# Optimization experiments

Hardware: AMD Instinct MI355X
Metric: run time of the kernel (lower is better)

## Reference

```python
import jax, jax.numpy as jnp
import numpy as np

N = 50000
E = 600000
FEAT = 32
ACT = 8
H = 128
HEADS = 4
C = H // HEADS
L = 3
NEG_SLOPE = 0.2
LN_EPS = 1e-5


def setup_inputs() -> dict:
    key = jax.random.key(0)
    ks = jax.random.split(key, 32)
    s = 0.05
    inp = {
        'x': jax.random.normal(ks[0], (N, FEAT), jnp.float32),
        'action': jax.random.normal(ks[1], (N, ACT), jnp.float32),
        'edge_index': jax.random.randint(ks[2], (2, E), 0, N, jnp.int32),
        # node encoder: Linear(feat+act -> H) + LayerNorm
        'W0': jax.random.normal(ks[3], (FEAT + ACT, H), jnp.float32) * s,
        'b0': jnp.zeros((H,), jnp.float32),
        'ln0_g': jnp.ones((H,), jnp.float32),
        'ln0_b': jnp.zeros((H,), jnp.float32),
        # GAT layers (stacked over L): lin W [L,H,heads*C], att vectors, bias, LayerNorm
        'Wg': jax.random.normal(ks[4], (L, H, HEADS * C), jnp.float32) * s,
        'att_src': jax.random.normal(ks[5], (L, HEADS, C), jnp.float32) * s,
        'att_dst': jax.random.normal(ks[6], (L, HEADS, C), jnp.float32) * s,
        'bg': jnp.zeros((L, HEADS * C), jnp.float32),
        'lng_g': jnp.ones((L, H), jnp.float32),
        'lng_b': jnp.zeros((L, H), jnp.float32),
        # dynamics head
        'Wd1': jax.random.normal(ks[7], (H, H), jnp.float32) * s,
        'bd1': jnp.zeros((H,), jnp.float32),
        'Wd2': jax.random.normal(ks[8], (H, FEAT), jnp.float32) * s,
        'bd2': jnp.zeros((FEAT,), jnp.float32),
        # reward head
        'Wr1': jax.random.normal(ks[9], (H, H // 2), jnp.float32) * s,
        'br1': jnp.zeros((H // 2,), jnp.float32),
        'Wr2': jax.random.normal(ks[10], (H // 2, 1), jnp.float32) * s,
        'br2': jnp.zeros((1,), jnp.float32),
        # constraint head
        'Wc1': jax.random.normal(ks[11], (H, H // 2), jnp.float32) * s,
        'bc1': jnp.zeros((H // 2,), jnp.float32),
        'Wc2': jax.random.normal(ks[12], (H // 2, 1), jnp.float32) * s,
        'bc2': jnp.zeros((1,), jnp.float32),
    }
    return inp


def _layernorm(x, g, b):
    mu = jnp.mean(x, axis=-1, keepdims=True)
    var = jnp.mean(jnp.square(x - mu), axis=-1, keepdims=True)
    return (x - mu) * jax.lax.rsqrt(var + LN_EPS) * g + b


def _gat_layer(h, src, dst, W, a_src, a_dst, bias):
    # PyG GATConv: xp = lin(h) per head; alpha = leaky_relu(a_src.x_j + a_dst.x_i)
    xp = (h @ W).reshape(N, HEADS, C)                    # [N, heads, C]
    s_src = jnp.sum(xp * a_src, axis=-1)                 # [N, heads]
    s_dst = jnp.sum(xp * a_dst, axis=-1)                 # [N, heads]
    alpha = jax.nn.leaky_relu(s_src[src] + s_dst[dst], NEG_SLOPE)  # [E', heads]
    # segment softmax over edges grouped by destination node
    amax = jax.ops.segment_max(alpha, dst, num_segments=N)
    ex = jnp.exp(alpha - amax[dst])
    den = jax.ops.segment_sum(ex, dst, num_segments=N)
    attn = ex / den[dst]                                 # [E', heads]
    msg = xp[src] * attn[..., None]                      # [E', heads, C]
    out = jax.ops.segment_sum(msg.reshape(-1, HEADS * C), dst, num_segments=N)
    return out + bias                                    # [N, H]


def reference(x, action, edge_index, W0, b0, ln0_g, ln0_b, Wg, att_src, att_dst,
              bg, lng_g, lng_b, Wd1, bd1, Wd2, bd2, Wr1, br1, Wr2, br2,
              Wc1, bc1, Wc2, bc2):
    # add self loops (PyG GATConv default)
    loops = jnp.arange(N, dtype=edge_index.dtype)
    src = jnp.concatenate([edge_index[0], loops])
    dst = jnp.concatenate([edge_index[1], loops])

    h = jax.nn.relu(_layernorm(jnp.concatenate([x, action], axis=-1) @ W0 + b0, ln0_g, ln0_b))
    for l in range(L):
        h_new = _gat_layer(h, src, dst, Wg[l], att_src[l], att_dst[l], bg[l])
        h_new = jax.nn.relu(_layernorm(h_new, lng_g[l], lng_b[l]))
        h = h + h_new

    delta_x = jax.nn.relu(h @ Wd1 + bd1) @ Wd2 + bd2
    next_x = x + delta_x
    graph_emb = jnp.mean(h, axis=0, keepdims=True)       # global_mean_pool, single graph
    reward = (jax.nn.relu(graph_emb @ Wr1 + br1) @ Wr2 + br2).squeeze(-1)
    constraint_prob = jax.nn.sigmoid(jax.nn.relu(graph_emb @ Wc1 + bc1) @ Wc2 + bc2).squeeze(-1)
    return delta_x, next_x, reward, constraint_prob
```

## Files before the change

kernel.cpp:

```cpp
#include <hip/hip_runtime.h>

typedef unsigned short u16;
typedef __attribute__((ext_vector_type(8))) short bf16x8;
typedef __attribute__((ext_vector_type(4))) float f32x4;

#define NN 50000
#define EE 600000
#define EP 650000
#define LNEPS 1e-5f
#define ENCB 1563
#define HB 2344
#define CNTB 2540
#define WTOT 93858
#define BSWN 65536
#define CW 64

__device__ __forceinline__ float bf2f(u16 u) {
    union { unsigned int i; float f; } v; v.i = ((unsigned int)u) << 16; return v.f;
}
__device__ __forceinline__ u16 f2bf(float f) {
    union { float f; unsigned int i; } v; v.f = f;
    unsigned int x = v.i;
    unsigned int r = x + 0x7fffu + ((x >> 16) & 1u);
    return (u16)(r >> 16);
}
__device__ __forceinline__ float ldf(const void* p, long i, int bf) {
    return bf ? bf2f(((const u16*)p)[i]) : ((const float*)p)[i];
}
__device__ __forceinline__ void stf(void* p, long i, int bf, float v) {
    if (bf) ((u16*)p)[i] = f2bf(v); else ((float*)p)[i] = v;
}

struct P22 { const void* p[22]; };

__global__ __launch_bounds__(256) void init7(P22 w, float* __restrict__ wf,
                                             u16* __restrict__ bsw,
                                             int* __restrict__ deg,
                                             float* __restrict__ gacc,
                                             int* __restrict__ flag) {
    const unsigned w0 = *(const unsigned*)w.p[2];
    const int bf = (w0 == 0x3F803F80u) ? 1 : 0;
    int i = blockIdx.x * 256 + threadIdx.x;
    if (i < WTOT) {
        const int offs[23] = {0,5120,5248,5376,5504,54656,55040,55424,55808,56192,56576,
                              72960,73088,77184,77216,85408,85472,85536,85537,93729,93793,
                              93857,93858};
        int seg = 0;
        while (offs[seg + 1] <= i) ++seg;
        wf[i] = ldf(w.p[seg], i - offs[seg], bf);
        return;
    }
    i -= WTOT;
    if (i < BSWN) {
        int mat = i >> 14, rem = i & 16383;
        int ct = rem >> 11, r2 = rem & 2047;
        int kb = r2 >> 9, r3 = r2 & 511;
        int lane = r3 >> 3, j = r3 & 7;
        int k = kb * 32 + (lane >> 4) * 8 + j;
        int n = ct * 16 + (lane & 15);
        float v = (mat < 3) ? ldf(w.p[4], (long)mat * 16384 + (long)k * 128 + n, bf)
                            : ldf(w.p[10], (long)k * 128 + n, bf);
        bsw[i] = f2bf(v);
        return;
    }
    i -= BSWN;
    if (i < NN) { deg[i] = 0; return; }
    i -= NN;
    if (i < 2048) { gacc[i] = 0.f; return; }
    if (i == 2048) *flag = bf;
}

__global__ __launch_bounds__(256) void enc9(
    const void* __restrict__ x, const void* __restrict__ act,
    const float* __restrict__ wf, u16* __restrict__ hb,
    const int* __restrict__ flg, const int* __restrict__ ei,
    int* __restrict__ deg, int* __restrict__ rank) {
    if (blockIdx.x >= ENCB) {
        int e = (blockIdx.x - ENCB) * 256 + threadIdx.x;
        if (e < EE) {
            int d = ei[EE + e];
            rank[e] = atomicAdd(&deg[d], 1);
        }
        return;
    }
    const float* W0f = wf;
    const float* b0f = wf + 5120;
    const float* gf  = wf + 5248;
    const float* bbf = wf + 5376;
    __shared__ float As[32][41];
    const int bf = *flg;
    int t = threadIdx.x;
    int r0 = blockIdx.x * 32;
    #pragma unroll
    for (int i = 0; i < 5; ++i) {
        int idx = t + i * 256;
        int r = idx / 40, k = idx - r * 40;
        int rr = r0 + r; if (rr >= NN) rr = NN - 1;
        As[r][k] = (k < 32) ? ldf(x, (long)rr * 32 + k, bf)
                            : ldf(act, (long)rr * 8 + (k - 32), bf);
    }
    __syncthreads();
    int colq = t & 31, mq = t >> 5;
    int col0 = colq * 4;
    float4 b0v = *(const float4*)(b0f + col0);
    float acc[4][4];
    #pragma unroll
    for (int j = 0; j < 4; ++j) {
        acc[j][0] = b0v.x; acc[j][1] = b0v.y; acc[j][2] = b0v.z; acc[j][3] = b0v.w;
    }
    #pragma unroll 2
    for (int k = 0; k < 40; ++k) {
        float4 b4 = *(const float4*)(W0f + k * 128 + col0);
        float a0 = As[mq * 4 + 0][k];
        float a1 = As[mq * 4 + 1][k];
        float a2 = As[mq * 4 + 2][k];
        float a3 = As[mq * 4 + 3][k];
        acc[0][0] += a0 * b4.x; acc[0][1] += a0 * b4.y; acc[0][2] += a0 * b4.z; acc[0][3] += a0 * b4.w;
        acc[1][0] += a1 * b4.x; acc[1][1] += a1 * b4.y; acc[1][2] += a1 * b4.z; acc[1][3] += a1 * b4.w;
        acc[2][0] += a2 * b4.x; acc[2][1] += a2 * b4.y; acc[2][2] += a2 * b4.z; acc[2][3] += a2 * b4.w;
        acc[3][0] += a3 * b4.x; acc[3][1] += a3 * b4.y; acc[3][2] += a3 * b4.z; acc[3][3] += a3 * b4.w;
    }
    float4 gv = *(const float4*)(gf + col0);
    float4 bv = *(const float4*)(bbf + col0);
    #pragma unroll
    for (int j = 0; j < 4; ++j) {
        int row = r0 + mq * 4 + j;
        float pa = acc[j][0] + acc[j][1] + acc[j][2] + acc[j][3];
        #pragma unroll
        for (int o = 1; o <= 16; o <<= 1) pa += __shfl_xor(pa, o, 32);
        float mu = pa * (1.f / 128.f);
        float d0 = acc[j][0] - mu, d1 = acc[j][1] - mu;
        float d2 = acc[j][2] - mu, d3 = acc[j][3] - mu;
        float q = d0 * d0 + d1 * d1 + d2 * d2 + d3 * d3;
        #pragma unroll
        for (int o = 1; o <= 16; o <<= 1) q += __shfl_xor(q, o, 32);
        float rs = rsqrtf(q * (1.f / 128.f) + LNEPS);
        if (row < NN) {
            ushort4 hbv;
            hbv.x = f2bf(fmaxf(d0 * rs * gv.x + bv.x, 0.f));
            hbv.y = f2bf(fmaxf(d1 * rs * gv.y + bv.y, 0.f));
            hbv.z = f2bf(fmaxf(d2 * rs * gv.z + bv.z, 0.f));
            hbv.w = f2bf(fmaxf(d3 * rs * gv.w + bv.w, 0.f));
            *(ushort4*)(hb + (long)row * 128 + col0) = hbv;
        }
    }
}

__global__ __launch_bounds__(256) void lin_score(
    const u16* __restrict__ hb, const u16* __restrict__ bswm,
    u16* __restrict__ out, const float* __restrict__ wf, int layer,
    float* __restrict__ s_src, float* __restrict__ s_dst,
    int doscatter, const int* __restrict__ ei, const int* __restrict__ rank,
    const int* __restrict__ deg, int* __restrict__ csrc) {
    if (doscatter && blockIdx.x >= ENCB) {
        int e = (blockIdx.x - ENCB) * 256 + threadIdx.x;
        if (e < EP) {
            if (e < EE) {
                int sv = ei[e], d = ei[EE + e];
                csrc[(long)d * CW + rank[e]] = sv;
            } else {
                int n = e - EE;
                csrc[(long)n * CW + deg[n]] = n;
            }
        }
        return;
    }
    __shared__ u16 As[32 * 136];
    int t = threadIdx.x;
    int r0 = blockIdx.x * 32;
    #pragma unroll
    for (int i = 0; i < 2; ++i) {
        int idx = (t + i * 256) * 8;
        int r = idx >> 7, k = idx & 127;
        int rr = r0 + r; if (rr >= NN) rr = NN - 1;
        int4 v = *(const int4*)(hb + (long)rr * 128 + k);
        *(int4*)(As + r * 136 + k) = v;
    }
    __syncthreads();
    int w = t >> 6, lane = t & 63;
    int rt = w & 1, ctbase = (w >> 1) * 4;
    int quad = lane >> 4, l15 = lane & 15;
    int rowl = rt * 16 + l15;
    bf16x8 afr[4];
    #pragma unroll
    for (int kb = 0; kb < 4; ++kb)
        afr[kb] = *(const bf16x8*)(As + rowl * 136 + kb * 32 + quad * 8);
    const float* asrf = wf + 54656 + layer * 128;
    const float* adsf = wf + 55040 + layer * 128;
    int headbase = (w >> 1) * 2;
    #pragma unroll
    for (int cp = 0; cp < 2; ++cp) {
        int ct0 = ctbase + cp * 2, ct1 = ct0 + 1;
        f32x4 acc0 = {0.f, 0.f, 0.f, 0.f};
        f32x4 acc1 = {0.f, 0.f, 0.f, 0.f};
        #pragma unroll
        for (int kb = 0; kb < 4; ++kb) {
            bf16x8 b0 = *(const bf16x8*)(bswm + ct0 * 2048 + kb * 512 + lane * 8);
            acc0 = __builtin_amdgcn_mfma_f32_16x16x32_bf16(afr[kb], b0, acc0, 0, 0, 0);
        }
        #pragma unroll
        for (int kb = 0; kb < 4; ++kb) {
            bf16x8 b1 = *(const bf16x8*)(bswm + ct1 * 2048 + kb * 512 + lane * 8);
            acc1 = __builtin_amdgcn_mfma_f32_16x16x32_bf16(afr[kb], b1, acc1, 0, 0, 0);
        }
        int col0 = ct0 * 16 + l15, col1 = ct1 * 16 + l15;
        #pragma unroll
        for (int reg = 0; reg < 4; ++reg) {
            int grow = r0 + rt * 16 + quad * 4 + reg;
            if (grow < NN) {
                out[(long)grow * 128 + col0] = f2bf(acc0[reg]);
                out[(long)grow * 128 + col1] = f2bf(acc1[reg]);
            }
        }
        float av0 = asrf[col0], av1 = asrf[col1];
        float dv0 = adsf[col0], dv1 = adsf[col1];
        #pragma unroll
        for (int reg = 0; reg < 4; ++reg) {
            float pa = acc0[reg] * av0 + acc1[reg] * av1;
            float pb = acc0[reg] * dv0 + acc1[reg] * dv1;
            #pragma unroll
            for (int o = 1; o <= 8; o <<= 1) {
                pa += __shfl_xor(pa, o, 64);
                pb += __shfl_xor(pb, o, 64);
            }
            if (l15 == 0) {
                int grow = r0 + rt * 16 + quad * 4 + reg;
                if (grow < NN) {
                    s_src[grow * 4 + headbase + cp] = pa;
                    s_dst[grow * 4 + headbase + cp] = pb;
                }
            }
        }
    }
}

__global__ __launch_bounds__(256) void lin_final(
    const u16* __restrict__ hb, const u16* __restrict__ bswm,
    const float* __restrict__ wf, const void* __restrict__ x,
    void* __restrict__ dout, const int* __restrict__ flg,
    float* __restrict__ gacc) {
    __shared__ u16 As[32 * 136];
    __shared__ u16 ts[32 * 136];
    __shared__ float ps[128];
    const float* bias = wf + 72960;
    int t = threadIdx.x;
    int r0 = blockIdx.x * 32;
    #pragma unroll
    for (int i = 0; i < 2; ++i) {
        int idx = (t + i * 256) * 8;
        int r = idx >> 7, k = idx & 127;
        int rr = r0 + r; if (rr >= NN) rr = NN - 1;
        int4 v = *(const int4*)(hb + (long)rr * 128 + k);
        *(int4*)(As + r * 136 + k) = v;
    }
    __syncthreads();
    int w = t >> 6, lane = t & 63;
    int rt = w & 1, ctbase = (w >> 1) * 4;
    int quad = lane >> 4, l15 = lane & 15;
    int rowl = rt * 16 + l15;
    bf16x8 afr[4];
    #pragma unroll
    for (int kb = 0; kb < 4; ++kb)
        afr[kb] = *(const bf16x8*)(As + rowl * 136 + kb * 32 + quad * 8);
    #pragma unroll
    for (int cp = 0; cp < 2; ++cp) {
        int ct0 = ctbase + cp * 2, ct1 = ct0 + 1;
        f32x4 acc0 = {0.f, 0.f, 0.f, 0.f};
        f32x4 acc1 = {0.f, 0.f, 0.f, 0.f};
        #pragma unroll
        for (int kb = 0; kb < 4; ++kb) {
            bf16x8 b0 = *(const bf16x8*)(bswm + ct0 * 2048 + kb * 512 + lane * 8);
            acc0 = __builtin_amdgcn_mfma_f32_16x16x32_bf16(afr[kb], b0, acc0, 0, 0, 0);
        }
        #pragma unroll
        for (int kb = 0; kb < 4; ++kb) {
            bf16x8 b1 = *(const bf16x8*)(bswm + ct1 * 2048 + kb * 512 + lane * 8);
            acc1 = __builtin_amdgcn_mfma_f32_16x16x32_bf16(afr[kb], b1, acc1, 0, 0, 0);
        }
        int col0 = ct0 * 16 + l15, col1 = ct1 * 16 + l15;
        float bia0 = bias[col0], bia1 = bias[col1];
        #pragma unroll
        for (int reg = 0; reg < 4; ++reg) {
            int lrow = rt * 16 + quad * 4 + reg;
            ts[lrow * 136 + col0] = f2bf(fmaxf(acc0[reg] + bia0, 0.f));
            ts[lrow * 136 + col1] = f2bf(fmaxf(acc1[reg] + bia1, 0.f));
        }
    }
    __syncthreads();
    const float* Wd2f = wf + 73088;
    const float* bd2f = wf + 77184;
    const int bf = *flg;
    int c = t & 31, mq = t >> 5;
    float acc[4];
    #pragma unroll
    for (int j = 0; j < 4; ++j) acc[j] = bd2f[c];
    #pragma unroll 4
    for (int k = 0; k < 128; ++k) {
        float wv = Wd2f[k * 32 + c];
        acc[0] += bf2f(ts[(mq * 4 + 0) * 136 + k]) * wv;
        acc[1] += bf2f(ts[(mq * 4 + 1) * 136 + k]) * wv;
        acc[2] += bf2f(ts[(mq * 4 + 2) * 136 + k]) * wv;
        acc[3] += bf2f(ts[(mq * 4 + 3) * 136 + k]) * wv;
    }
    #pragma unroll
    for (int j = 0; j < 4; ++j) {
        int node = r0 + mq * 4 + j;
        if (node >= NN) continue;
        stf(dout, (long)node * 32 + c, bf, acc[j]);
        stf(dout, (long)NN * 32 + (long)node * 32 + c, bf,
            ldf(x, (long)node * 32 + c, bf) + acc[j]);
    }
    int pc = t & 127, half = t >> 7;
    float s = 0.f;
    #pragma unroll
    for (int r2 = half * 16; r2 < half * 16 + 16; ++r2) {
        if (r0 + r2 < NN) s += bf2f(As[r2 * 136 + pc]);
    }
    if (half == 0) ps[pc] = s;
    __syncthreads();
    if (half == 1) atomicAdd(&gacc[(blockIdx.x & 15) * 128 + pc], s + ps[pc]);
}

__global__ __launch_bounds__(128) void head5(
    const float* __restrict__ gacc, const float* __restrict__ wf,
    void* __restrict__ out, const int* __restrict__ flg) {
    const float* Wr1f = wf + 77216;
    const float* br1f = wf + 85408;
    const float* Wr2f = wf + 85472;
    const float* br2f = wf + 85536;
    const float* Wc1f = wf + 85537;
    const float* bc1f = wf + 93729;
    const float* Wc2f = wf + 93793;
    const float* bc2f = wf + 93857;
    __shared__ float ge[128];
    __shared__ float hr[128];
    const int bf = *flg;
    int t = threadIdx.x;
    {
        float s = 0.f;
        #pragma unroll
        for (int k2 = 0; k2 < 16; ++k2) s += gacc[k2 * 128 + t];
        ge[t] = s * (1.f / (float)NN);
    }
    __syncthreads();
    {
        int j = t & 63;
        const float* W = (t < 64) ? Wr1f : Wc1f;
        const float* bb = (t < 64) ? br1f : bc1f;
        float a = bb[j];
        for (int k = 0; k < 128; ++k) a += ge[k] * W[k * 64 + j];
        hr[t] = fmaxf(a, 0.f);
    }
    __syncthreads();
    if (t == 0) {
        float r = br2f[0];
        for (int j = 0; j < 64; ++j) r += hr[j] * Wr2f[j];
        stf(out, (long)2 * NN * 32, bf, r);
    } else if (t == 1) {
        float z = bc2f[0];
        for (int j = 0; j < 64; ++j) z += hr[64 + j] * Wc2f[j];
        float p = 1.f / (1.f + __expf(-z));
        stf(out, (long)2 * NN * 32 + 1, bf, p);
    }
}

__global__ __launch_bounds__(256) void agg11(
    const u16* __restrict__ xp, const float* __restrict__ s_src,
    const float* __restrict__ s_dst,
    const int* __restrict__ csrc, const int* __restrict__ deg,
    const float* __restrict__ wf, int layer, u16* __restrict__ hb) {
    const float* bgf = wf + 55424 + layer * 128;
    const float* gf  = wf + 55808 + layer * 128;
    const float* bbf = wf + 56192 + layer * 128;
    int t = threadIdx.x;
    int lane = t & 63;
    int n = blockIdx.x * 4 + (t >> 6);
    int q = (lane >> 4) & 3;
    int l16 = lane & 15;
    int c0 = l16 * 8;
    int hd = l16 >> 2;
    long idx0 = (long)n * 128 + c0;
    int4 hold = *(const int4*)(hb + idx0);
    float sdn = s_dst[n * 4 + (lane & 3)];
    int cdeg = deg[n] + 1;
    if (cdeg > CW) cdeg = CW;
    int eidx = (lane < cdeg) ? csrc[(long)n * CW + lane] : n;
    float a[8] = {};
    float den = 0.f;
    for (int base = 0; base < cdeg; base += 16) {
        int me = base + (lane >> 2);
        int sm = __shfl(eidx, me & 63, 64);
        float aw = s_src[sm * 4 + (lane & 3)] + sdn;
        aw = (aw > 0.f) ? aw : 0.2f * aw;
        float wv = (me < cdeg) ? __expf(aw) : 0.f;
        int s00 = __shfl(eidx, base + q, 64);
        int s01 = __shfl(eidx, base + 4 + q, 64);
        int s10 = __shfl(eidx, base + 8 + q, 64);
        int s11 = __shfl(eidx, base + 12 + q, 64);
        int4 v00 = *(const int4*)(xp + (long)s00 * 128 + c0);
        int4 v01 = *(const int4*)(xp + (long)s01 * 128 + c0);
        int4 v10 = *(const int4*)(xp + (long)s10 * 128 + c0);
        int4 v11 = *(const int4*)(xp + (long)s11 * 128 + c0);
        float w00 = __shfl(wv, (q << 2) | hd, 64);
        float w01 = __shfl(wv, ((4 + q) << 2) | hd, 64);
        float w10 = __shfl(wv, ((8 + q) << 2) | hd, 64);
        float w11 = __shfl(wv, ((12 + q) << 2) | hd, 64);
        union { int4 i; u16 u[8]; } u00, u01, u10, u11;
        u00.i = v00; u01.i = v01; u10.i = v10; u11.i = v11;
        #pragma unroll
        for (int k = 0; k < 8; ++k)
            a[k] += w00 * bf2f(u00.u[k]) + w01 * bf2f(u01.u[k])
                  + w10 * bf2f(u10.u[k]) + w11 * bf2f(u11.u[k]);
        den += w00 + w01 + w10 + w11;
    }
    #pragma unroll
    for (int k = 0; k < 8; ++k) {
        a[k] += __shfl_xor(a[k], 16, 64);
        a[k] += __shfl_xor(a[k], 32, 64);
    }
    den += __shfl_xor(den, 16, 64);
    den += __shfl_xor(den, 32, 64);
    float inv = 1.f / den;
    float4 bg0 = *(const float4*)(bgf + c0);
    float4 bg1 = *(const float4*)(bgf + c0 + 4);
    float v[8];
    v[0] = a[0] * inv + bg0.x; v[1] = a[1] * inv + bg0.y;
    v[2] = a[2] * inv + bg0.z; v[3] = a[3] * inv + bg0.w;
    v[4] = a[4] * inv + bg1.x; v[5] = a[5] * inv + bg1.y;
    v[6] = a[6] * inv + bg1.z; v[7] = a[7] * inv + bg1.w;
    float pa = v[0] + v[1] + v[2] + v[3] + v[4] + v[5] + v[6] + v[7];
    #pragma unroll
    for (int o = 1; o <= 8; o <<= 1) pa += __shfl_xor(pa, o, 16);
    float mu = pa * (1.f / 128.f);
    float d[8];
    float qv = 0.f;
    #pragma unroll
    for (int k = 0; k < 8; ++k) { d[k] = v[k] - mu; qv += d[k] * d[k]; }
    #pragma unroll
    for (int o = 1; o <= 8; o <<= 1) qv += __shfl_xor(qv, o, 16);
    float rs = rsqrtf(qv * (1.f / 128.f) + LNEPS);
    float4 g0 = *(const float4*)(gf + c0);
    float4 g1 = *(const float4*)(gf + c0 + 4);
    float4 b0 = *(const float4*)(bbf + c0);
    float4 b1 = *(const float4*)(bbf + c0 + 4);
    float gg[8]  = {g0.x, g0.y, g0.z, g0.w, g1.x, g1.y, g1.z, g1.w};
    float bbv[8] = {b0.x, b0.y, b0.z, b0.w, b1.x, b1.y, b1.z, b1.w};
    if (lane < 16) {
        union { int4 i; u16 u[8]; } hv, ho;
        ho.i = hold;
        #pragma unroll
        for (int k = 0; k < 8; ++k) {
            float y = fmaxf(d[k] * rs * gg[k] + bbv[k], 0.f);
            hv.u[k] = f2bf(bf2f(ho.u[k]) + y);
        }
        *(int4*)(hb + idx0) = hv.i;
    }
}

extern "C" void kernel_launch(void* const* d_in, const int* in_sizes, int n_in,
                              void* d_out, int out_size, void* d_ws, size_t ws_size,
                              hipStream_t stream) {
    const void* x   = d_in[0];
    const void* act = d_in[1];
    const int*  ei  = (const int*)d_in[2];

    char* ws = (char*)d_ws;
    size_t off = 0;
    auto alloc = [&](size_t bytes) -> char* {
        char* p = ws + off;
        off = (off + bytes + 255) & ~(size_t)255;
        return p;
    };
    u16*       hb     = (u16*)   alloc((size_t)NN * 128 * 2);
    u16*       xp     = (u16*)   alloc((size_t)NN * 128 * 2);
    float*     s_src  = (float*) alloc((size_t)NN * 4 * 4);
    float*     s_dst  = (float*) alloc((size_t)NN * 4 * 4);
    int*       deg    = (int*)   alloc((size_t)NN * 4);
    int*       rank   = (int*)   alloc((size_t)EE * 4);
    int*       csrc   = (int*)   alloc((size_t)NN * CW * 4);
    float*     wf     = (float*) alloc((size_t)WTOT * 4);
    u16*       bsw    = (u16*)   alloc((size_t)BSWN * 2);
    float*     gacc   = (float*) alloc(16 * 128 * 4);
    int*       flag   = (int*)   alloc(4);

    P22 wp;
    for (int i = 0; i < 22; ++i) wp.p[i] = d_in[3 + i];

    const int initN = WTOT + BSWN + NN + 2048 + 1;
    init7<<<(initN + 255) / 256, 256, 0, stream>>>(wp, wf, bsw, deg, gacc, flag);

    enc9<<<ENCB + HB, 256, 0, stream>>>(x, act, wf, hb, flag, ei, deg, rank);

    for (int l = 0; l < 3; ++l) {
        int grid = (l == 0) ? (ENCB + CNTB) : ENCB;
        lin_score<<<grid, 256, 0, stream>>>(hb, bsw + (size_t)l * 16384, xp,
                                            wf, l, s_src, s_dst,
                                            (l == 0) ? 1 : 0, ei, rank, deg,
                                            csrc);
        agg11<<<NN / 4, 256, 0, stream>>>(xp, s_src, s_dst, csrc, deg,
                                          wf, l, hb);
    }

    lin_final<<<ENCB, 256, 0, stream>>>(hb, bsw + (size_t)3 * 16384,
                                        wf, x, d_out, flag, gacc);

    head5<<<1, 128, 0, stream>>>(gacc, wf, d_out, flag);

    (void)in_sizes; (void)n_in; (void)out_size; (void)ws_size;
}
```

Measured before the change: 339.7 us.

## Fuse GAT aggregation with next layer's linear+score into one kernel

Each GAT layer's edge aggregation, LayerNorm and residual update now run in the same kernel as the next layer's projection and attention-score GEMM. The aggregated row tile stays in shared memory as the MFMA A operand instead of being re-read from global memory. The final layer aggregation is fused the same way into the output-head kernel. Ping-pong xp/score buffers keep concurrent blocks from reading and writing the same projected features. Aggregation now runs with 32 rows per block over 1563 blocks, eight rows per wave in sequence, so there is less parallelism for hiding gather latency than the previous 4-nodes-per-block launch.

```diff
diff --git a/kernel.cpp b/kernel.cpp
--- a/kernel.cpp
+++ b/kernel.cpp
@@ -146,6 +146,109 @@
     }
 }
 
+
+__device__ __forceinline__ void agg_phase(
+    const u16* __restrict__ xp, const float* __restrict__ s_src,
+    const float* __restrict__ s_dst, const int* __restrict__ csrc,
+    const int* __restrict__ deg, const float* __restrict__ wf, int layer,
+    u16* __restrict__ hb, u16* __restrict__ As) {
+    const float* bgf = wf + 55424 + layer * 128;
+    const float* gf  = wf + 55808 + layer * 128;
+    const float* bbf = wf + 56192 + layer * 128;
+    int t = threadIdx.x;
+    int lane = t & 63;
+    int w = t >> 6;
+    int r0 = blockIdx.x * 32;
+    int q = (lane >> 4) & 3;
+    int l16 = lane & 15;
+    int c0 = l16 * 8;
+    int hd = l16 >> 2;
+    for (int i = 0; i < 8; ++i) {
+        int lrow = w * 8 + i;
+        int n = r0 + lrow;
+        if (n >= NN) {
+            if (lane < 16) { int4 z = {0, 0, 0, 0}; *(int4*)(As + lrow * 136 + c0) = z; }
+            continue;
+        }
+        long idx0 = (long)n * 128 + c0;
+        int4 hold = *(const int4*)(hb + idx0);
+        float sdn = s_dst[n * 4 + (lane & 3)];
+        int cdeg = deg[n] + 1; if (cdeg > CW) cdeg = CW;
+        int eidx = (lane < cdeg) ? csrc[(long)n * CW + lane] : n;
+        float a[8] = {};
+        float den = 0.f;
+        for (int base = 0; base < cdeg; base += 16) {
+            int me = base + (lane >> 2);
+            int sm = __shfl(eidx, me & 63, 64);
+            float aw = s_src[sm * 4 + (lane & 3)] + sdn;
+            aw = (aw > 0.f) ? aw : 0.2f * aw;
+            float wv = (me < cdeg) ? __expf(aw) : 0.f;
+            int s00 = __shfl(eidx, base + q, 64);
+            int s01 = __shfl(eidx, base + 4 + q, 64);
+            int s10 = __shfl(eidx, base + 8 + q, 64);
+            int s11 = __shfl(eidx, base + 12 + q, 64);
+            int4 v00 = *(const int4*)(xp + (long)s00 * 128 + c0);
+            int4 v01 = *(const int4*)(xp + (long)s01 * 128 + c0);
+            int4 v10 = *(const int4*)(xp + (long)s10 * 128 + c0);
+            int4 v11 = *(const int4*)(xp + (long)s11 * 128 + c0);
+            float w00 = __shfl(wv, (q << 2) | hd, 64);
+            float w01 = __shfl(wv, ((4 + q) << 2) | hd, 64);
+            float w10 = __shfl(wv, ((8 + q) << 2) | hd, 64);
+            float w11 = __shfl(wv, ((12 + q) << 2) | hd, 64);
+            union { int4 i; u16 u[8]; } u00, u01, u10, u11;
+            u00.i = v00; u01.i = v01; u10.i = v10; u11.i = v11;
+            #pragma unroll
+            for (int k = 0; k < 8; ++k)
+                a[k] += w00 * bf2f(u00.u[k]) + w01 * bf2f(u01.u[k])
+                      + w10 * bf2f(u10.u[k]) + w11 * bf2f(u11.u[k]);
+            den += w00 + w01 + w10 + w11;
+        }
+        #pragma unroll
+        for (int k = 0; k < 8; ++k) {
+            a[k] += __shfl_xor(a[k], 16, 64);
+            a[k] += __shfl_xor(a[k], 32, 64);
+        }
+        den += __shfl_xor(den, 16, 64);
+        den += __shfl_xor(den, 32, 64);
+        float inv = 1.f / den;
+        float4 bg0 = *(const float4*)(bgf + c0);
+        float4 bg1 = *(const float4*)(bgf + c0 + 4);
+        float v[8];
+        v[0] = a[0] * inv + bg0.x; v[1] = a[1] * inv + bg0.y;
+        v[2] = a[2] * inv + bg0.z; v[3] = a[3] * inv + bg0.w;
+        v[4] = a[4] * inv + bg1.x; v[5] = a[5] * inv + bg1.y;
+        v[6] = a[6] * inv + bg1.z; v[7] = a[7] * inv + bg1.w;
+        float pa = v[0] + v[1] + v[2] + v[3] + v[4] + v[5] + v[6] + v[7];
+        #pragma unroll
+        for (int o = 1; o <= 8; o <<= 1) pa += __shfl_xor(pa, o, 16);
+        float mu = pa * (1.f / 128.f);
+        float d[8];
+        float qv = 0.f;
+        #pragma unroll
+        for (int k = 0; k < 8; ++k) { d[k] = v[k] - mu; qv += d[k] * d[k]; }
+        #pragma unroll
+        for (int o = 1; o <= 8; o <<= 1) qv += __shfl_xor(qv, o, 16);
+        float rs = rsqrtf(qv * (1.f / 128.f) + LNEPS);
+        float4 g0 = *(const float4*)(gf + c0);
+        float4 g1 = *(const float4*)(gf + c0 + 4);
+        float4 b0 = *(const float4*)(bbf + c0);
+        float4 b1 = *(const float4*)(bbf + c0 + 4);
+        float gg[8]  = {g0.x, g0.y, g0.z, g0.w, g1.x, g1.y, g1.z, g1.w};
+        float bbv[8] = {b0.x, b0.y, b0.z, b0.w, b1.x, b1.y, b1.z, b1.w};
+        if (lane < 16) {
+            union { int4 i; u16 u[8]; } hv, ho;
+            ho.i = hold;
+            #pragma unroll
+            for (int k = 0; k < 8; ++k) {
+                float y = fmaxf(d[k] * rs * gg[k] + bbv[k], 0.f);
+                hv.u[k] = f2bf(bf2f(ho.u[k]) + y);
+            }
+            *(int4*)(hb + idx0) = hv.i;
+            *(int4*)(As + lrow * 136 + c0) = hv.i;
+        }
+    }
+}
+
 __global__ __launch_bounds__(256) void lin_score(
     const u16* __restrict__ hb, const u16* __restrict__ bswm,
     u16* __restrict__ out, const float* __restrict__ wf, int layer,
@@ -234,26 +337,91 @@
     }
 }
 
-__global__ __launch_bounds__(256) void lin_final(
-    const u16* __restrict__ hb, const u16* __restrict__ bswm,
-    const float* __restrict__ wf, const void* __restrict__ x,
-    void* __restrict__ dout, const int* __restrict__ flg,
-    float* __restrict__ gacc) {
+__global__ __launch_bounds__(256) void fal(
+    const u16* __restrict__ xp_in, const float* __restrict__ ss_in,
+    const float* __restrict__ sd_in, const int* __restrict__ csrc,
+    const int* __restrict__ deg, const float* __restrict__ wf, int la,
+    u16* __restrict__ hb, const u16* __restrict__ bswm,
+    u16* __restrict__ xp_out, float* __restrict__ ss_out,
+    float* __restrict__ sd_out) {
+    __shared__ u16 As[32 * 136];
+    agg_phase(xp_in, ss_in, sd_in, csrc, deg, wf, la, hb, As);
+    __syncthreads();
+    int t = threadIdx.x;
+    int r0 = blockIdx.x * 32;
+    int lb = la + 1;
+    int w = t >> 6, lane = t & 63;
+    int rt = w & 1, ctbase = (w >> 1) * 4;
+    int quad = lane >> 4, l15 = lane & 15;
+    int rowl = rt * 16 + l15;
+    bf16x8 afr[4];
+    #pragma unroll
+    for (int kb = 0; kb < 4; ++kb)
+        afr[kb] = *(const bf16x8*)(As + rowl * 136 + kb * 32 + quad * 8);
+    const float* asrf = wf + 54656 + lb * 128;
+    const float* adsf = wf + 55040 + lb * 128;
+    int headbase = (w >> 1) * 2;
+    #pragma unroll
+    for (int cp = 0; cp < 2; ++cp) {
+        int ct0 = ctbase + cp * 2, ct1 = ct0 + 1;
+        f32x4 acc0 = {0.f, 0.f, 0.f, 0.f};
+        f32x4 acc1 = {0.f, 0.f, 0.f, 0.f};
+        #pragma unroll
+        for (int kb = 0; kb < 4; ++kb) {
+            bf16x8 b0 = *(const bf16x8*)(bswm + ct0 * 2048 + kb * 512 + lane * 8);
+            acc0 = __builtin_amdgcn_mfma_f32_16x16x32_bf16(afr[kb], b0, acc0, 0, 0, 0);
+        }
+        #pragma unroll
+        for (int kb = 0; kb < 4; ++kb) {
+            bf16x8 b1 = *(const bf16x8*)(bswm + ct1 * 2048 + kb * 512 + lane * 8);
+            acc1 = __builtin_amdgcn_mfma_f32_16x16x32_bf16(afr[kb], b1, acc1, 0, 0, 0);
+        }
+        int col0 = ct0 * 16 + l15, col1 = ct1 * 16 + l15;
+        #pragma unroll
+        for (int reg = 0; reg < 4; ++reg) {
+            int grow = r0 + rt * 16 + quad * 4 + reg;
+            if (grow < NN) {
+                xp_out[(long)grow * 128 + col0] = f2bf(acc0[reg]);
+                xp_out[(long)grow * 128 + col1] = f2bf(acc1[reg]);
+            }
+        }
+        float av0 = asrf[col0], av1 = asrf[col1];
+        float dv0 = adsf[col0], dv1 = adsf[col1];
+        #pragma unroll
+        for (int reg = 0; reg < 4; ++reg) {
+            float pa = acc0[reg] * av0 + acc1[reg] * av1;
+            float pb = acc0[reg] * dv0 + acc1[reg] * dv1;
+            #pragma unroll
+            for (int o = 1; o <= 8; o <<= 1) {
+                pa += __shfl_xor(pa, o, 64);
+                pb += __shfl_xor(pb, o, 64);
+            }
+            if (l15 == 0) {
+                int grow = r0 + rt * 16 + quad * 4 + reg;
+                if (grow < NN) {
+                    ss_out[grow * 4 + headbase + cp] = pa;
+                    sd_out[grow * 4 + headbase + cp] = pb;
+                }
+            }
+        }
+    }
+}
+
+__global__ __launch_bounds__(256) void falf(
+    const u16* __restrict__ xp_in, const float* __restrict__ ss_in,
+    const float* __restrict__ sd_in, const int* __restrict__ csrc,
+    const int* __restrict__ deg, const float* __restrict__ wf,
+    u16* __restrict__ hb, const u16* __restrict__ bswm,
+    const void* __restrict__ x, void* __restrict__ dout,
+    const int* __restrict__ flg, float* __restrict__ gacc) {
     __shared__ u16 As[32 * 136];
     __shared__ u16 ts[32 * 136];
     __shared__ float ps[128];
+    agg_phase(xp_in, ss_in, sd_in, csrc, deg, wf, 2, hb, As);
+    __syncthreads();
     const float* bias = wf + 72960;
     int t = threadIdx.x;
     int r0 = blockIdx.x * 32;
-    #pragma unroll
-    for (int i = 0; i < 2; ++i) {
-        int idx = (t + i * 256) * 8;
-        int r = idx >> 7, k = idx & 127;
-        int rr = r0 + r; if (rr >= NN) rr = NN - 1;
-        int4 v = *(const int4*)(hb + (long)rr * 128 + k);
-        *(int4*)(As + r * 136 + k) = v;
-    }
-    __syncthreads();
     int w = t >> 6, lane = t & 63;
     int rt = w & 1, ctbase = (w >> 1) * 4;
     int quad = lane >> 4, l15 = lane & 15;
@@ -364,99 +532,6 @@
     }
 }
 
-__global__ __launch_bounds__(256) void agg11(
-    const u16* __restrict__ xp, const float* __restrict__ s_src,
-    const float* __restrict__ s_dst,
-    const int* __restrict__ csrc, const int* __restrict__ deg,
-    const float* __restrict__ wf, int layer, u16* __restrict__ hb) {
-    const float* bgf = wf + 55424 + layer * 128;
-    const float* gf  = wf + 55808 + layer * 128;
-    const float* bbf = wf + 56192 + layer * 128;
-    int t = threadIdx.x;
-    int lane = t & 63;
-    int n = blockIdx.x * 4 + (t >> 6);
-    int q = (lane >> 4) & 3;
-    int l16 = lane & 15;
-    int c0 = l16 * 8;
-    int hd = l16 >> 2;
-    long idx0 = (long)n * 128 + c0;
-    int4 hold = *(const int4*)(hb + idx0);
-    float sdn = s_dst[n * 4 + (lane & 3)];
-    int cdeg = deg[n] + 1;
-    if (cdeg > CW) cdeg = CW;
-    int eidx = (lane < cdeg) ? csrc[(long)n * CW + lane] : n;
-    float a[8] = {};
-    float den = 0.f;
-    for (int base = 0; base < cdeg; base += 16) {
-        int me = base + (lane >> 2);
-        int sm = __shfl(eidx, me & 63, 64);
-        float aw = s_src[sm * 4 + (lane & 3)] + sdn;
-        aw = (aw > 0.f) ? aw : 0.2f * aw;
-        float wv = (me < cdeg) ? __expf(aw) : 0.f;
-        int s00 = __shfl(eidx, base + q, 64);
-        int s01 = __shfl(eidx, base + 4 + q, 64);
-        int s10 = __shfl(eidx, base + 8 + q, 64);
-        int s11 = __shfl(eidx, base + 12 + q, 64);
-        int4 v00 = *(const int4*)(xp + (long)s00 * 128 + c0);
-        int4 v01 = *(const int4*)(xp + (long)s01 * 128 + c0);
-        int4 v10 = *(const int4*)(xp + (long)s10 * 128 + c0);
-        int4 v11 = *(const int4*)(xp + (long)s11 * 128 + c0);
-        float w00 = __shfl(wv, (q << 2) | hd, 64);
-        float w01 = __shfl(wv, ((4 + q) << 2) | hd, 64);
-        float w10 = __shfl(wv, ((8 + q) << 2) | hd, 64);
-        float w11 = __shfl(wv, ((12 + q) << 2) | hd, 64);
-        union { int4 i; u16 u[8]; } u00, u01, u10, u11;
-        u00.i = v00; u01.i = v01; u10.i = v10; u11.i = v11;
-        #pragma unroll
-        for (int k = 0; k < 8; ++k)
-            a[k] += w00 * bf2f(u00.u[k]) + w01 * bf2f(u01.u[k])
-                  + w10 * bf2f(u10.u[k]) + w11 * bf2f(u11.u[k]);
-        den += w00 + w01 + w10 + w11;
-    }
-    #pragma unroll
-    for (int k = 0; k < 8; ++k) {
-        a[k] += __shfl_xor(a[k], 16, 64);
-        a[k] += __shfl_xor(a[k], 32, 64);
-    }
-    den += __shfl_xor(den, 16, 64);
-    den += __shfl_xor(den, 32, 64);
-    float inv = 1.f / den;
-    float4 bg0 = *(const float4*)(bgf + c0);
-    float4 bg1 = *(const float4*)(bgf + c0 + 4);
-    float v[8];
-    v[0] = a[0] * inv + bg0.x; v[1] = a[1] * inv + bg0.y;
-    v[2] = a[2] * inv + bg0.z; v[3] = a[3] * inv + bg0.w;
-    v[4] = a[4] * inv + bg1.x; v[5] = a[5] * inv + bg1.y;
-    v[6] = a[6] * inv + bg1.z; v[7] = a[7] * inv + bg1.w;
-    float pa = v[0] + v[1] + v[2] + v[3] + v[4] + v[5] + v[6] + v[7];
-    #pragma unroll
-    for (int o = 1; o <= 8; o <<= 1) pa += __shfl_xor(pa, o, 16);
-    float mu = pa * (1.f / 128.f);
-    float d[8];
-    float qv = 0.f;
-    #pragma unroll
-    for (int k = 0; k < 8; ++k) { d[k] = v[k] - mu; qv += d[k] * d[k]; }
-    #pragma unroll
-    for (int o = 1; o <= 8; o <<= 1) qv += __shfl_xor(qv, o, 16);
-    float rs = rsqrtf(qv * (1.f / 128.f) + LNEPS);
-    float4 g0 = *(const float4*)(gf + c0);
-    float4 g1 = *(const float4*)(gf + c0 + 4);
-    float4 b0 = *(const float4*)(bbf + c0);
-    float4 b1 = *(const float4*)(bbf + c0 + 4);
-    float gg[8]  = {g0.x, g0.y, g0.z, g0.w, g1.x, g1.y, g1.z, g1.w};
-    float bbv[8] = {b0.x, b0.y, b0.z, b0.w, b1.x, b1.y, b1.z, b1.w};
-    if (lane < 16) {
-        union { int4 i; u16 u[8]; } hv, ho;
-        ho.i = hold;
-        #pragma unroll
-        for (int k = 0; k < 8; ++k) {
-            float y = fmaxf(d[k] * rs * gg[k] + bbv[k], 0.f);
-            hv.u[k] = f2bf(bf2f(ho.u[k]) + y);
-        }
-        *(int4*)(hb + idx0) = hv.i;
-    }
-}
-
 extern "C" void kernel_launch(void* const* d_in, const int* in_sizes, int n_in,
                               void* d_out, int out_size, void* d_ws, size_t ws_size,
                               hipStream_t stream) {
@@ -472,9 +547,12 @@
         return p;
     };
     u16*       hb     = (u16*)   alloc((size_t)NN * 128 * 2);
-    u16*       xp     = (u16*)   alloc((size_t)NN * 128 * 2);
-    float*     s_src  = (float*) alloc((size_t)NN * 4 * 4);
-    float*     s_dst  = (float*) alloc((size_t)NN * 4 * 4);
+    u16*       xpA    = (u16*)   alloc((size_t)NN * 128 * 2);
+    u16*       xpB    = (u16*)   alloc((size_t)NN * 128 * 2);
+    float*     ssA    = (float*) alloc((size_t)NN * 4 * 4);
+    float*     sdA    = (float*) alloc((size_t)NN * 4 * 4);
+    float*     ssB    = (float*) alloc((size_t)NN * 4 * 4);
+    float*     sdB    = (float*) alloc((size_t)NN * 4 * 4);
     int*       deg    = (int*)   alloc((size_t)NN * 4);
     int*       rank   = (int*)   alloc((size_t)EE * 4);
     int*       csrc   = (int*)   alloc((size_t)NN * CW * 4);
@@ -491,18 +569,16 @@
 
     enc9<<<ENCB + HB, 256, 0, stream>>>(x, act, wf, hb, flag, ei, deg, rank);
 
-    for (int l = 0; l < 3; ++l) {
-        int grid = (l == 0) ? (ENCB + CNTB) : ENCB;
-        lin_score<<<grid, 256, 0, stream>>>(hb, bsw + (size_t)l * 16384, xp,
-                                            wf, l, s_src, s_dst,
-                                            (l == 0) ? 1 : 0, ei, rank, deg,
-                                            csrc);
-        agg11<<<NN / 4, 256, 0, stream>>>(xp, s_src, s_dst, csrc, deg,
-                                          wf, l, hb);
-    }
-
-    lin_final<<<ENCB, 256, 0, stream>>>(hb, bsw + (size_t)3 * 16384,
-                                        wf, x, d_out, flag, gacc);
+    lin_score<<<ENCB + CNTB, 256, 0, stream>>>(hb, bsw, xpA,
+                                               wf, 0, ssA, sdA,
+                                               1, ei, rank, deg, csrc);
+
+    fal<<<ENCB, 256, 0, stream>>>(xpA, ssA, sdA, csrc, deg, wf, 0, hb,
+                                  bsw + (size_t)1 * 16384, xpB, ssB, sdB);
+    fal<<<ENCB, 256, 0, stream>>>(xpB, ssB, sdB, csrc, deg, wf, 1, hb,
+                                  bsw + (size_t)2 * 16384, xpA, ssA, sdA);
+    falf<<<ENCB, 256, 0, stream>>>(xpA, ssA, sdA, csrc, deg, wf, hb,
+                                   bsw + (size_t)3 * 16384, x, d_out, flag, gacc);
 
     head5<<<1, 128, 0, stream>>>(gacc, wf, d_out, flag);
 
```

Result: slower. 361.6 us (+6.5%).
